# Kernel tuning notes

Hardware: AMD Instinct MI355X
Metric: run time of the kernel (lower is better)

Reference implementation:

```python
import jax, jax.numpy as jnp
import numpy as np

N_USERS = 100000
N_GAMES = 20000
D_USER = 128
D_GAME = 64
EMB = 64
H = 256
E = 1000000
S = 500000


def setup_inputs() -> dict:
    key = jax.random.key(0)
    ks = jax.random.split(key, 32)

    def w(k, fi, fo):
        return jax.random.normal(k, (fi, fo), jnp.float32) / np.float32(np.sqrt(fi))

    d_game_full = D_GAME + EMB  # game features concat game embedding
    inp = {
        "x_user": jax.random.normal(ks[0], (N_USERS, D_USER), jnp.float32),
        "x_game": jax.random.normal(ks[1], (N_GAMES, D_GAME), jnp.float32),
        "emb_game": jax.random.normal(ks[2], (N_GAMES, EMB), jnp.float32) * 0.1,
        "edge_weight_ug": jax.random.uniform(ks[3], (E,), jnp.float32),
        "edge_weight_gu": jax.random.uniform(ks[4], (E,), jnp.float32),
        "src_ug": jax.random.randint(ks[5], (E,), 0, N_USERS, jnp.int32),
        "dst_ug": jax.random.randint(ks[6], (E,), 0, N_GAMES, jnp.int32),
        "src_gu": jax.random.randint(ks[7], (E,), 0, N_GAMES, jnp.int32),
        "dst_gu": jax.random.randint(ks[8], (E,), 0, N_USERS, jnp.int32),
        "score_row": jax.random.randint(ks[9], (S,), 0, N_USERS, jnp.int32),
        "score_col": jax.random.randint(ks[10], (S,), 0, N_GAMES, jnp.int32),
    }
    # GraphConv params per layer per edge type: W_rel (messages), bias, W_root (self)
    dims = [(D_USER, d_game_full, H), (H, H, H), (H, H, H)]
    i = 11
    for l, (du, dg, out) in enumerate(dims, 1):
        inp[f"W_rel_ug{l}"] = w(ks[i], du, out); i += 1
        inp[f"b_ug{l}"] = jnp.zeros((out,), jnp.float32)
        inp[f"W_root_g{l}"] = w(ks[i], dg, out); i += 1
        inp[f"W_rel_gu{l}"] = w(ks[i], dg, out); i += 1
        inp[f"b_gu{l}"] = jnp.zeros((out,), jnp.float32)
        inp[f"W_root_u{l}"] = w(ks[i], du, out); i += 1
    return inp


def reference(x_user, x_game, emb_game, edge_weight_ug, edge_weight_gu,
              W_rel_ug1, b_ug1, W_root_g1, W_rel_gu1, b_gu1, W_root_u1,
              W_rel_ug2, b_ug2, W_root_g2, W_rel_gu2, b_gu2, W_root_u2,
              W_rel_ug3, b_ug3, W_root_g3, W_rel_gu3, b_gu3, W_root_u3,
              src_ug, dst_ug, src_gu, dst_gu, score_row, score_col):
    def conv(x_src, x_dst, src, dst, ew, Wr, br, Wo, n_dst):
        # GraphConv: sum_j w_ij * x_j -> lin_rel, plus lin_root(x_i)
        msg = jax.ops.segment_sum(x_src[src] * ew[:, None], dst, num_segments=n_dst)
        return msg @ Wr + br + x_dst @ Wo

    xu = x_user                                   # [Nu, 128]
    xg = jnp.concatenate([x_game, emb_game], axis=1)  # [Ng, 128]

    g = jax.nn.relu(conv(xu, xg, src_ug, dst_ug, edge_weight_ug, W_rel_ug1, b_ug1, W_root_g1, N_GAMES))
    u = jax.nn.relu(conv(xg, xu, src_gu, dst_gu, edge_weight_gu, W_rel_gu1, b_gu1, W_root_u1, N_USERS))

    g2 = jax.nn.relu(conv(u, g, src_ug, dst_ug, edge_weight_ug, W_rel_ug2, b_ug2, W_root_g2, N_GAMES))
    u2 = jax.nn.relu(conv(g, u, src_gu, dst_gu, edge_weight_gu, W_rel_gu2, b_gu2, W_root_u2, N_USERS))

    g3 = conv(u2, g2, src_ug, dst_ug, edge_weight_ug, W_rel_ug3, b_ug3, W_root_g3, N_GAMES)
    u3 = conv(g2, u2, src_gu, dst_gu, edge_weight_gu, W_rel_gu3, b_gu3, W_root_u3, N_USERS)
    # dropout(0.2) in eval mode is identity

    # DotProductEdgeDecoder
    return jnp.sum(u3[score_row] * g3[score_col], axis=1)  # [S]
```

## Files before the change

### kernel.cpp

```cpp
#include <hip/hip_runtime.h>

typedef unsigned short bf16_t;
typedef __attribute__((ext_vector_type(8))) short bf16x8;
typedef __attribute__((ext_vector_type(4))) float f32x4;

static constexpr int NU = 100000;
static constexpr int NG = 20000;
static constexpr int HD = 256;
static constexpr int EE = 1000000;
static constexpr int SS = 500000;

static constexpr int SH_G = 6,  SPAN_G = 64;
static constexpr int SH_U = 7,  SPAN_U = 128;
static constexpr int BKT_G = (NG + SPAN_G - 1) / SPAN_G;
static constexpr int BKT_U = (NU + SPAN_U - 1) / SPAN_U;
static constexpr int CAP_G = 4096;
static constexpr int CAP_U = 2048;
static constexpr int NBMAX = 1024;
static constexpr int PA_BLOCKS = 256;
static constexpr int PA_CHUNK = (EE + PA_BLOCKS - 1) / PA_BLOCKS;
static constexpr int TILE = 4096;

__device__ __forceinline__ float b2f(bf16_t u) {
    union { unsigned int i; float f; } x; x.i = ((unsigned int)u) << 16; return x.f;
}
__device__ __forceinline__ bf16_t f2b(float f) {
    union { float f; unsigned int i; } x; x.f = f;
    unsigned int r = x.i + 0x7FFF + ((x.i >> 16) & 1);
    return (bf16_t)(r >> 16);
}

__device__ __forceinline__ void accum8(float* acc, uint4 r, float w) {
    unsigned int u[4] = {r.x, r.y, r.z, r.w};
#pragma unroll
    for (int i = 0; i < 4; i++) {
        float lo = __uint_as_float(u[i] << 16);
        float hi = __uint_as_float(u[i] & 0xFFFF0000u);
        acc[2 * i]     = fmaf(w, lo, acc[2 * i]);
        acc[2 * i + 1] = fmaf(w, hi, acc[2 * i + 1]);
    }
}

__global__ void prep_feats(const float* __restrict__ xgame, const float* __restrict__ emb,
                           const float* __restrict__ xuser,
                           bf16_t* __restrict__ xg, bf16_t* __restrict__ xu,
                           int* __restrict__ gcg, int* __restrict__ gcu) {
    int id = blockIdx.x * 256 + threadIdx.x;
    if (id < BKT_G) gcg[id] = 0;
    if (id < BKT_U) gcu[id] = 0;
    const int ng4 = NG * 32;
    if (id < ng4) {
        int r = id >> 5, c = (id & 31) * 4;
        float4 v = (c < 64) ? *(const float4*)&xgame[(size_t)r * 64 + c]
                            : *(const float4*)&emb[(size_t)r * 64 + (c - 64)];
        ((ushort4*)xg)[id] = make_ushort4(f2b(v.x), f2b(v.y), f2b(v.z), f2b(v.w));
    } else {
        int j = id - ng4;
        if (j >= NU * 32) return;
        float4 v = ((const float4*)xuser)[j];
        ((ushort4*)xu)[j] = make_ushort4(f2b(v.x), f2b(v.y), f2b(v.z), f2b(v.w));
    }
}

struct WtArgs {
    const float* src[12];
    bf16_t* dst[12];
    int K[12];
    int off[13];
};
__global__ void wt_all(WtArgs a, int total) {
    int id = blockIdx.x * 256 + threadIdx.x;
    if (id >= total) return;
    int s = 0;
    while (id >= a.off[s + 1]) ++s;
    int local = id - a.off[s];
    int K = a.K[s];
    int k = local >> 8, n = local & 255;
    a.dst[s][(size_t)n * K + k] = f2b(a.src[s][local]);
}

__global__ __launch_bounds__(256) void chisto(const int* __restrict__ dug,
                                              const int* __restrict__ dgu,
                                              int* __restrict__ gcg, int* __restrict__ gcu) {
    __shared__ int cnt[NBMAX];
    int blk = blockIdx.x;
    int dir = blk >> 8, lb = blk & 255;
    const int* dst = dir ? dgu : dug;
    int* gc = dir ? gcu : gcg;
    int B = dir ? BKT_U : BKT_G;
    int sh = dir ? SH_U : SH_G;
    int t = threadIdx.x;
    for (int i = t; i < NBMAX; i += 256) cnt[i] = 0;
    __syncthreads();
    int beg = lb * PA_CHUNK, fin = min(EE, beg + PA_CHUNK);
    for (int i = beg + t; i < fin; i += 256)
        atomicAdd(&cnt[((unsigned)dst[i]) >> sh], 1);
    __syncthreads();
    for (int i = t; i < B; i += 256)
        if (cnt[i]) atomicAdd(&gc[i], cnt[i]);
}

__global__ void scan_coarse(const int* __restrict__ gcg, const int* __restrict__ gcu,
                            int* __restrict__ baseg, int* __restrict__ baseu,
                            int* __restrict__ gcurg, int* __restrict__ gcuru,
                            int* __restrict__ rpg, int* __restrict__ rpu) {
    if (blockIdx.x == 0 && threadIdx.x == 0) {
        int run = 0;
        for (int i = 0; i < BKT_G; i++) { baseg[i] = run; gcurg[i] = run; run += gcg[i]; }
        rpg[NG] = EE;
    } else if (blockIdx.x == 1 && threadIdx.x == 0) {
        int run = 0;
        for (int i = 0; i < BKT_U; i++) { baseu[i] = run; gcuru[i] = run; run += gcu[i]; }
        rpu[NU] = EE;
    }
}

__global__ __launch_bounds__(256) void passA(
    const int* __restrict__ sug, const int* __restrict__ dug, const float* __restrict__ wug,
    const int* __restrict__ sgu, const int* __restrict__ dgu, const float* __restrict__ wgu,
    int* __restrict__ gcurg, int* __restrict__ gcuru,
    int2* __restrict__ tmpG, int2* __restrict__ tmpU) {
    __shared__ int cnt[NBMAX], sscan[NBMAX], gb[NBMAX], sd[256];
    __shared__ unsigned short rankArr[TILE], sbkt[TILE];
    __shared__ int2 staged[TILE];
    int blk = blockIdx.x;
    int dir = blk >> 8, lb = blk & 255;
    const int* src = dir ? sgu : sug;
    const int* dst = dir ? dgu : dug;
    const float* w = dir ? wgu : wug;
    int* gcur = dir ? gcuru : gcurg;
    int2* tmp = dir ? tmpU : tmpG;
    int B = dir ? BKT_U : BKT_G;
    int sh = dir ? SH_U : SH_G;
    unsigned lmask = dir ? (SPAN_U - 1) : (SPAN_G - 1);
    int t = threadIdx.x;
    int beg = lb * PA_CHUNK, fin = min(EE, beg + PA_CHUNK);
    int n = fin - beg;
    for (int i = t; i < NBMAX; i += 256) cnt[i] = 0;
    __syncthreads();
    for (int i = t; i < n; i += 256) {
        int bkt = ((unsigned)dst[beg + i]) >> sh;
        rankArr[i] = (unsigned short)atomicAdd(&cnt[bkt], 1);
    }
    __syncthreads();
    {
        int v[4]; int s = 0;
#pragma unroll
        for (int j = 0; j < 4; j++) { v[j] = cnt[t * 4 + j]; s += v[j]; }
        sd[t] = s;
        __syncthreads();
        for (int off = 1; off < 256; off <<= 1) {
            int y = (t >= off) ? sd[t - off] : 0;
            __syncthreads();
            sd[t] += y;
            __syncthreads();
        }
        int run = sd[t] - s;
#pragma unroll
        for (int j = 0; j < 4; j++) { sscan[t * 4 + j] = run; run += v[j]; }
    }
    __syncthreads();
    for (int i = t; i < n; i += 256) {
        unsigned d = (unsigned)dst[beg + i];
        int bkt = d >> sh;
        int pos = sscan[bkt] + rankArr[i];
        staged[pos] = make_int2(src[beg + i] | ((d & lmask) << 17), __float_as_int(w[beg + i]));
        sbkt[pos] = (unsigned short)bkt;
    }
    __syncthreads();
    for (int i = t; i < B; i += 256)
        if (cnt[i]) gb[i] = atomicAdd(&gcur[i], cnt[i]);
    __syncthreads();
    for (int i = t; i < n; i += 256) {
        int bkt = sbkt[i];
        tmp[gb[bkt] + i - sscan[bkt]] = staged[i];
    }
}

template <int SPANB, int CAP>
__global__ __launch_bounds__(256) void passB(
    const int2* __restrict__ tmp, const int* __restrict__ base,
    int* __restrict__ rowptr, int2* __restrict__ eout, int B, int ntot) {
    __shared__ int cnt2[SPANB], lexcl[SPANB], cur[SPANB];
    __shared__ int2 staged[CAP];
    constexpr int KMAX = CAP / 256;
    int bkt = blockIdx.x;
    if (bkt >= B) return;
    int start = base[bkt];
    int end = (bkt == B - 1) ? EE : base[bkt + 1];
    int row0 = bkt * SPANB;
    int t = threadIdx.x;
    int count = end - start;
    if (count <= CAP) {
        for (int i = t; i < SPANB; i += 256) cnt2[i] = 0;
        __syncthreads();
        int2 e[KMAX]; int rk[KMAX];
#pragma unroll
        for (int k = 0; k < KMAX; k++) {
            int i = t + k * 256;
            if (i < count) {
                e[k] = tmp[start + i];
                rk[k] = atomicAdd(&cnt2[((unsigned)e[k].x) >> 17], 1);
            }
        }
        __syncthreads();
        if (t == 0) {
            int run = 0;
            for (int r = 0; r < SPANB; r++) { lexcl[r] = run; run += cnt2[r]; }
        }
        __syncthreads();
#pragma unroll
        for (int k = 0; k < KMAX; k++) {
            int i = t + k * 256;
            if (i < count) {
                int r = ((unsigned)e[k].x) >> 17;
                staged[lexcl[r] + rk[k]] = e[k];
            }
        }
        __syncthreads();
        for (int r = t; r < SPANB; r += 256) {
            int row = row0 + r;
            if (row < ntot) rowptr[row] = start + lexcl[r];
        }
        for (int i = t; i < count; i += 256) {
            int2 s = staged[i];
            eout[start + i] = make_int2(s.x & 0x1FFFF, s.y);
        }
    } else {
        for (int i = t; i < SPANB; i += 256) cnt2[i] = 0;
        __syncthreads();
        for (int i = start + t; i < end; i += 256)
            atomicAdd(&cnt2[((unsigned)tmp[i].x) >> 17], 1);
        __syncthreads();
        if (t == 0) {
            int run = 0;
            for (int r = 0; r < SPANB; r++) { int v = cnt2[r]; cur[r] = run; run += v; }
        }
        __syncthreads();
        for (int r = t; r < SPANB; r += 256) {
            int row = row0 + r;
            if (row < ntot) rowptr[row] = start + cur[r];
        }
        __syncthreads();
        for (int pos = start; pos < end; pos += CAP) {
            int n = min(CAP, end - pos);
            for (int i = t; i < SPANB; i += 256) cnt2[i] = 0;
            __syncthreads();
            int2 e[KMAX]; int rk[KMAX];
#pragma unroll
            for (int k = 0; k < KMAX; k++) {
                int i = t + k * 256;
                if (i < n) {
                    e[k] = tmp[pos + i];
                    rk[k] = atomicAdd(&cnt2[((unsigned)e[k].x) >> 17], 1);
                }
            }
            __syncthreads();
            if (t == 0) {
                int run = 0;
                for (int r = 0; r < SPANB; r++) { lexcl[r] = run; run += cnt2[r]; }
            }
            __syncthreads();
#pragma unroll
            for (int k = 0; k < KMAX; k++) {
                int i = t + k * 256;
                if (i < n) {
                    int r = ((unsigned)e[k].x) >> 17;
                    staged[lexcl[r] + rk[k]] = e[k];
                }
            }
            __syncthreads();
            for (int i = t; i < n; i += 256) {
                int2 s = staged[i];
                int r = ((unsigned)s.x) >> 17;
                int g = start + cur[r] + (i - lexcl[r]);
                eout[g] = make_int2(s.x & 0x1FFFF, s.y);
            }
            __syncthreads();
            for (int r = t; r < SPANB; r += 256) cur[r] += cnt2[r];
            __syncthreads();
        }
    }
}

template <int D>
__global__ __launch_bounds__(256) void seg_sum16(
    const bf16_t* __restrict__ feat, const int* __restrict__ rowptr,
    const int2* __restrict__ edges, bf16_t* __restrict__ out, int n_rows) {
    constexpr int LPE = D / 8;
    constexpr int EP = 64 / LPE;
    constexpr int UN = 4;
    int wid = (blockIdx.x * 256 + threadIdx.x) >> 6;
    int lane = threadIdx.x & 63;
    if (wid >= n_rows) return;
    int beg = rowptr[wid], end = rowptr[wid + 1];
    const int h = lane / LPE;
    const int cl = lane % LPE;
    const uint4* fb = (const uint4*)feat;
    float acc[8] = {};
    for (int eb = beg; eb < end; eb += UN * EP) {
        int2 ed[UN]; bool v[UN]; uint4 r[UN];
#pragma unroll
        for (int u = 0; u < UN; u++) {
            int e = eb + u * EP + h;
            v[u] = e < end;
            ed[u] = edges[v[u] ? e : beg];
        }
#pragma unroll
        for (int u = 0; u < UN; u++)
            r[u] = fb[(size_t)ed[u].x * (D / 8) + cl];
#pragma unroll
        for (int u = 0; u < UN; u++)
            accum8(acc, r[u], v[u] ? __int_as_float(ed[u].y) : 0.f);
    }
#pragma unroll
    for (int k = 0; k < 8; ++k) {
        acc[k] += __shfl_down(acc[k], 32, 64);
        if (LPE == 16) acc[k] += __shfl_down(acc[k], 16, 64);
    }
    if (lane < LPE) {
        uint4 o;
        o.x = (unsigned)f2b(acc[0]) | ((unsigned)f2b(acc[1]) << 16);
        o.y = (unsigned)f2b(acc[2]) | ((unsigned)f2b(acc[3]) << 16);
        o.z = (unsigned)f2b(acc[4]) | ((unsigned)f2b(acc[5]) << 16);
        o.w = (unsigned)f2b(acc[6]) | ((unsigned)f2b(acc[7]) << 16);
        ((uint4*)(out + (size_t)wid * D))[lane] = o;
    }
}

template <bool TWOPASS>
__global__ __launch_bounds__(256) void gemm_mfma(
    const bf16_t* __restrict__ A1, const bf16_t* __restrict__ W1t,
    const bf16_t* __restrict__ A2, const bf16_t* __restrict__ W2t,
    const float* __restrict__ bias, bf16_t* __restrict__ C,
    int M, int K, int addc, int relu) {
    constexpr int LS = 40;
    __shared__ bf16_t As[128 * LS];
    __shared__ bf16_t Bs[128 * LS];
    const int t = threadIdx.x;
    const int lane = t & 63, wave = t >> 6;
    const int wm = (wave >> 1) * 64, wn = (wave & 1) * 64;
    const int rowBase = blockIdx.x * 128;
    const int colBase = blockIdx.y * 128;
    const int lm = lane & 15;
    const int quad = lane >> 4;
    f32x4 acc[4][4] = {};

    const int npass = TWOPASS ? 2 : 1;
    for (int pass = 0; pass < npass; ++pass) {
        const bf16_t* A = pass ? A2 : A1;
        const bf16_t* Wt = pass ? W2t : W1t;
        for (int k0 = 0; k0 < K; k0 += 32) {
#pragma unroll
            for (int i = 0; i < 2; ++i) {
                int li = t + i * 256;
                int r = li >> 2, c = (li & 3) * 8;
                int gm = rowBase + r;
                bf16x8 v = {};
                if (gm < M) v = *(const bf16x8*)&A[(size_t)gm * K + k0 + c];
                *(bf16x8*)&As[r * LS + c] = v;
            }
#pragma unroll
            for (int i = 0; i < 2; ++i) {
                int li = t + i * 256;
                int r = li >> 2, c = (li & 3) * 8;
                bf16x8 v = *(const bf16x8*)&Wt[(size_t)(colBase + r) * K + k0 + c];
                *(bf16x8*)&Bs[r * LS + c] = v;
            }
            __syncthreads();
            bf16x8 af[4], bfr[4];
#pragma unroll
            for (int i = 0; i < 4; ++i)
                af[i] = *(const bf16x8*)&As[(wm + i * 16 + lm) * LS + quad * 8];
#pragma unroll
            for (int j = 0; j < 4; ++j)
                bfr[j] = *(const bf16x8*)&Bs[(wn + j * 16 + lm) * LS + quad * 8];
#pragma unroll
            for (int i = 0; i < 4; ++i)
#pragma unroll
                for (int j = 0; j < 4; ++j)
                    acc[i][j] = __builtin_amdgcn_mfma_f32_16x16x32_bf16(bfr[j], af[i], acc[i][j], 0, 0, 0);
            __syncthreads();
        }
    }

#pragma unroll
    for (int i = 0; i < 4; ++i) {
        int row = rowBase + wm + i * 16 + lm;
        if (row >= M) continue;
#pragma unroll
        for (int j = 0; j < 4; ++j) {
            int col = colBase + wn + j * 16 + quad * 4;
            float v0 = acc[i][j][0], v1 = acc[i][j][1], v2 = acc[i][j][2], v3 = acc[i][j][3];
            if (bias) {
                float4 b4 = *(const float4*)&bias[col];
                v0 += b4.x; v1 += b4.y; v2 += b4.z; v3 += b4.w;
            }
            bf16_t* cp = &C[(size_t)row * HD + col];
            if (addc) {
                ushort4 old = *(const ushort4*)cp;
                v0 += b2f(old.x); v1 += b2f(old.y); v2 += b2f(old.z); v3 += b2f(old.w);
            }
            if (relu) {
                v0 = fmaxf(v0, 0.f); v1 = fmaxf(v1, 0.f);
                v2 = fmaxf(v2, 0.f); v3 = fmaxf(v3, 0.f);
            }
            *(ushort4*)cp = make_ushort4(f2b(v0), f2b(v1), f2b(v2), f2b(v3));
        }
    }
}

__global__ __launch_bounds__(256) void decode2(
    const bf16_t* __restrict__ u3, const bf16_t* __restrict__ g3,
    const int* __restrict__ row, const int* __restrict__ col,
    float* __restrict__ out, int S) {
    int wid = (blockIdx.x * 256 + threadIdx.x) >> 6;
    int lane = threadIdx.x & 63;
    int p = wid * 2 + (lane >> 5);
    int cl = lane & 31;
    if (p >= S) p = S - 1;
    int r = row[p], c = col[p];
    uint4 a = ((const uint4*)(u3 + (size_t)r * 256))[cl];
    uint4 b = ((const uint4*)(g3 + (size_t)c * 256))[cl];
    float s = 0.f;
    unsigned ua[4] = {a.x, a.y, a.z, a.w}, ub[4] = {b.x, b.y, b.z, b.w};
#pragma unroll
    for (int i = 0; i < 4; i++) {
        float alo = __uint_as_float(ua[i] << 16), ahi = __uint_as_float(ua[i] & 0xFFFF0000u);
        float blo = __uint_as_float(ub[i] << 16), bhi = __uint_as_float(ub[i] & 0xFFFF0000u);
        s = fmaf(alo, blo, s);
        s = fmaf(ahi, bhi, s);
    }
#pragma unroll
    for (int d = 16; d > 0; d >>= 1) s += __shfl_down(s, d, 64);
    if (cl == 0) out[p] = s;
}

extern "C" void kernel_launch(void* const* d_in, const int* in_sizes, int n_in,
                              void* d_out, int out_size, void* d_ws, size_t ws_size,
                              hipStream_t stream) {
    const float* x_user  = (const float*)d_in[0];
    const float* x_game  = (const float*)d_in[1];
    const float* emb_game= (const float*)d_in[2];
    const float* ew_ug   = (const float*)d_in[3];
    const float* ew_gu   = (const float*)d_in[4];
    const int* src_ug    = (const int*)d_in[5];
    const int* dst_ug    = (const int*)d_in[6];
    const int* src_gu    = (const int*)d_in[7];
    const int* dst_gu    = (const int*)d_in[8];
    const int* score_row = (const int*)d_in[9];
    const int* score_col = (const int*)d_in[10];
    const float* Wr_ug[3] = {(const float*)d_in[11], (const float*)d_in[17], (const float*)d_in[23]};
    const float* b_ug[3]  = {(const float*)d_in[12], (const float*)d_in[18], (const float*)d_in[24]};
    const float* Wo_g[3]  = {(const float*)d_in[13], (const float*)d_in[19], (const float*)d_in[25]};
    const float* Wr_gu[3] = {(const float*)d_in[14], (const float*)d_in[20], (const float*)d_in[26]};
    const float* b_gu[3]  = {(const float*)d_in[15], (const float*)d_in[21], (const float*)d_in[27]};
    const float* Wo_u[3]  = {(const float*)d_in[16], (const float*)d_in[22], (const float*)d_in[28]};
    float* out = (float*)d_out;
    (void)in_sizes; (void)n_in; (void)out_size;

    constexpr size_t WS_NEEDED = 183500000;
    if (ws_size < WS_NEEDED) return;

    char* ws = (char*)d_ws;
    size_t off = 0;
    auto alloc = [&](size_t bytes) -> void* {
        void* p = ws + off;
        off += (bytes + 255) & ~(size_t)255;
        return p;
    };
    bf16_t* xg   = (bf16_t*)alloc((size_t)NG * 128 * 2);
    bf16_t* xu   = (bf16_t*)alloc((size_t)NU * 128 * 2);
    bf16_t* uA   = (bf16_t*)alloc((size_t)NU * HD * 2);
    bf16_t* uB   = (bf16_t*)alloc((size_t)NU * HD * 2);
    bf16_t* gA   = (bf16_t*)alloc((size_t)NG * HD * 2);
    bf16_t* gB   = (bf16_t*)alloc((size_t)NG * HD * 2);
    bf16_t* buf  = (bf16_t*)alloc((size_t)NG * HD * 2);
    int2*   e_ug = (int2*)  alloc((size_t)EE * 8);
    int2*   e_gu = (int2*)  alloc((size_t)EE * 8);
    bf16_t* WrugT[3], *WogT[3], *WrguT[3], *WouT[3];
    const int Ks[3] = {128, 256, 256};
    for (int l = 0; l < 3; ++l) {
        WrugT[l] = (bf16_t*)alloc((size_t)Ks[l] * HD * 2);
        WogT[l]  = (bf16_t*)alloc((size_t)Ks[l] * HD * 2);
        WrguT[l] = (bf16_t*)alloc((size_t)Ks[l] * HD * 2);
        WouT[l]  = (bf16_t*)alloc((size_t)Ks[l] * HD * 2);
    }
    int* rowptr_g = (int*)alloc((NG + 1) * 4);
    int* rowptr_u = (int*)alloc((NU + 1) * 4);
    int* gcnt_g   = (int*)alloc(BKT_G * 4);
    int* gcnt_u   = (int*)alloc(BKT_U * 4);
    int* base_g   = (int*)alloc(BKT_G * 4);
    int* base_u   = (int*)alloc(BKT_U * 4);
    int* gcur_g   = (int*)alloc(BKT_G * 4);
    int* gcur_u   = (int*)alloc(BKT_U * 4);
    int2* tmp_g = (int2*)uB;
    int2* tmp_u = tmp_g + EE;

    {
        int n4 = NG * 32 + NU * 32;
        prep_feats<<<(n4 + 255) / 256, 256, 0, stream>>>(x_game, emb_game, x_user, xg, xu,
                                                         gcnt_g, gcnt_u);
        WtArgs wa;
        const float* srcs[12] = {Wr_ug[0], Wo_g[0], Wr_gu[0], Wo_u[0],
                                 Wr_ug[1], Wo_g[1], Wr_gu[1], Wo_u[1],
                                 Wr_ug[2], Wo_g[2], Wr_gu[2], Wo_u[2]};
        bf16_t* dsts[12] = {WrugT[0], WogT[0], WrguT[0], WouT[0],
                            WrugT[1], WogT[1], WrguT[1], WouT[1],
                            WrugT[2], WogT[2], WrguT[2], WouT[2]};
        int total = 0;
        for (int i = 0; i < 12; ++i) {
            wa.src[i] = srcs[i]; wa.dst[i] = dsts[i];
            wa.K[i] = Ks[i / 4]; wa.off[i] = total;
            total += Ks[i / 4] * HD;
        }
        wa.off[12] = total;
        wt_all<<<(total + 255) / 256, 256, 0, stream>>>(wa, total);
    }
    chisto<<<2 * PA_BLOCKS, 256, 0, stream>>>(dst_ug, dst_gu, gcnt_g, gcnt_u);
    scan_coarse<<<2, 64, 0, stream>>>(gcnt_g, gcnt_u, base_g, base_u, gcur_g, gcur_u,
                                      rowptr_g, rowptr_u);
    passA<<<2 * PA_BLOCKS, 256, 0, stream>>>(src_ug, dst_ug, ew_ug, src_gu, dst_gu, ew_gu,
                                             gcur_g, gcur_u, tmp_g, tmp_u);
    passB<SPAN_G, CAP_G><<<BKT_G, 256, 0, stream>>>(tmp_g, base_g, rowptr_g, e_ug, BKT_G, NG);
    passB<SPAN_U, CAP_U><<<BKT_U, 256, 0, stream>>>(tmp_u, base_u, rowptr_u, e_gu, BKT_U, NU);

    const dim3 GG((NG + 127) / 128, 2), GU((NU + 127) / 128, 2);
    const int SEG_G = (NG + 3) / 4, SEG_U = (NU + 3) / 4;

    seg_sum16<128><<<SEG_G, 256, 0, stream>>>(xu, rowptr_g, e_ug, buf, NG);
    gemm_mfma<true><<<GG, 256, 0, stream>>>(buf, WrugT[0], xg, WogT[0], b_ug[0], gA, NG, 128, 0, 1);
    gemm_mfma<false><<<GG, 256, 0, stream>>>(xg, WrguT[0], nullptr, nullptr, nullptr, buf, NG, 128, 0, 0);
    seg_sum16<256><<<SEG_U, 256, 0, stream>>>(buf, rowptr_u, e_gu, uA, NU);
    gemm_mfma<false><<<GU, 256, 0, stream>>>(xu, WouT[0], nullptr, nullptr, b_gu[0], uA, NU, 128, 1, 1);

    seg_sum16<256><<<SEG_G, 256, 0, stream>>>(uA, rowptr_g, e_ug, buf, NG);
    gemm_mfma<true><<<GG, 256, 0, stream>>>(buf, WrugT[1], gA, WogT[1], b_ug[1], gB, NG, 256, 0, 1);
    gemm_mfma<false><<<GG, 256, 0, stream>>>(gA, WrguT[1], nullptr, nullptr, nullptr, buf, NG, 256, 0, 0);
    seg_sum16<256><<<SEG_U, 256, 0, stream>>>(buf, rowptr_u, e_gu, uB, NU);
    gemm_mfma<false><<<GU, 256, 0, stream>>>(uA, WouT[1], nullptr, nullptr, b_gu[1], uB, NU, 256, 1, 1);

    seg_sum16<256><<<SEG_G, 256, 0, stream>>>(uB, rowptr_g, e_ug, buf, NG);
    gemm_mfma<true><<<GG, 256, 0, stream>>>(buf, WrugT[2], gB, WogT[2], b_ug[2], gA, NG, 256, 0, 0);
    gemm_mfma<false><<<GG, 256, 0, stream>>>(gB, WrguT[2], nullptr, nullptr, nullptr, buf, NG, 256, 0, 0);
    seg_sum16<256><<<SEG_U, 256, 0, stream>>>(buf, rowptr_u, e_gu, uA, NU);
    gemm_mfma<false><<<GU, 256, 0, stream>>>(uB, WouT[2], nullptr, nullptr, b_gu[2], uA, NU, 256, 1, 0);

    decode2<<<((SS + 1) / 2 + 3) / 4, 256, 0, stream>>>(uA, gA, score_row, score_col, out, SS);
}
```

Measured before the change: 931.7 us.

## Fuse independent game-side GEMMs with segment-sum launches via block-index dispatch

Turns the segment-sum and GEMM kernels into device bodies and adds a combined kernel that sends the first blocks to a GEMM and the rest to a segment sum. Each game-side GEMM now runs concurrently with an independent aggregation in the same launch, with intermediate buffers reassigned to existing storage (gB and xu) to avoid write conflicts. The aim is to fill idle compute units during the small GEMMs and drop launch gaps. In exchange, segment-sum blocks inherit the GEMM's shared-memory and register footprint, which could lower their occupancy.

New measurement: 1.036 ms. 11.2% more time.

```diff
diff --git a/kernel.cpp b/kernel.cpp
--- a/kernel.cpp
+++ b/kernel.cpp
@@ -284,13 +284,13 @@
 }
 
 template <int D>
-__global__ __launch_bounds__(256) void seg_sum16(
+__device__ __forceinline__ void seg_body(
     const bf16_t* __restrict__ feat, const int* __restrict__ rowptr,
-    const int2* __restrict__ edges, bf16_t* __restrict__ out, int n_rows) {
+    const int2* __restrict__ edges, bf16_t* __restrict__ out, int n_rows, int blk) {
     constexpr int LPE = D / 8;
     constexpr int EP = 64 / LPE;
     constexpr int UN = 4;
-    int wid = (blockIdx.x * 256 + threadIdx.x) >> 6;
+    int wid = (blk * 256 + (int)threadIdx.x) >> 6;
     int lane = threadIdx.x & 63;
     if (wid >= n_rows) return;
     int beg = rowptr[wid], end = rowptr[wid + 1];
@@ -329,19 +329,19 @@
 }
 
 template <bool TWOPASS>
-__global__ __launch_bounds__(256) void gemm_mfma(
+__device__ __forceinline__ void gemm_body(
     const bf16_t* __restrict__ A1, const bf16_t* __restrict__ W1t,
     const bf16_t* __restrict__ A2, const bf16_t* __restrict__ W2t,
     const float* __restrict__ bias, bf16_t* __restrict__ C,
-    int M, int K, int addc, int relu) {
+    int M, int K, int addc, int relu, int bx, int by) {
     constexpr int LS = 40;
     __shared__ bf16_t As[128 * LS];
     __shared__ bf16_t Bs[128 * LS];
     const int t = threadIdx.x;
     const int lane = t & 63, wave = t >> 6;
     const int wm = (wave >> 1) * 64, wn = (wave & 1) * 64;
-    const int rowBase = blockIdx.x * 128;
-    const int colBase = blockIdx.y * 128;
+    const int rowBase = bx * 128;
+    const int colBase = by * 128;
     const int lm = lane & 15;
     const int quad = lane >> 4;
     f32x4 acc[4][4] = {};
@@ -408,6 +408,28 @@
             *(ushort4*)cp = make_ushort4(f2b(v0), f2b(v1), f2b(v2), f2b(v3));
         }
     }
+}
+
+template <bool TWOPASS>
+__global__ __launch_bounds__(256) void gemm_mfma(
+    const bf16_t* A1, const bf16_t* W1t, const bf16_t* A2, const bf16_t* W2t,
+    const float* bias, bf16_t* C, int M, int K, int addc, int relu) {
+    gemm_body<TWOPASS>(A1, W1t, A2, W2t, bias, C, M, K, addc, relu, blockIdx.x, blockIdx.y);
+}
+
+template <int D, bool TWOPASS>
+__global__ __launch_bounds__(256) void fused_gs(
+    const bf16_t* A1, const bf16_t* W1t, const bf16_t* A2, const bf16_t* W2t,
+    const float* bias, bf16_t* C, int M, int K, int addc, int relu,
+    int gemmBlocks, int gridM,
+    const bf16_t* feat, const int* rowptr, const int2* edges,
+    bf16_t* segOut, int n_rows) {
+    int b = blockIdx.x;
+    if (b < gemmBlocks)
+        gemm_body<TWOPASS>(A1, W1t, A2, W2t, bias, C, M, K, addc, relu,
+                           b % gridM, b / gridM);
+    else
+        seg_body<D>(feat, rowptr, edges, segOut, n_rows, b - gemmBlocks);
 }
 
 __global__ __launch_bounds__(256) void decode2(
@@ -496,6 +518,8 @@
     int* gcur_u   = (int*)alloc(BKT_U * 4);
     int2* tmp_g = (int2*)uB;
     int2* tmp_u = tmp_g + EE;
+    bf16_t* Ybuf1 = gB;
+    bf16_t* Ybuf23 = xu;
 
     {
         int n4 = NG * 32 + NU * 32;
@@ -525,26 +549,37 @@
     passB<SPAN_G, CAP_G><<<BKT_G, 256, 0, stream>>>(tmp_g, base_g, rowptr_g, e_ug, BKT_G, NG);
     passB<SPAN_U, CAP_U><<<BKT_U, 256, 0, stream>>>(tmp_u, base_u, rowptr_u, e_gu, BKT_U, NU);
 
-    const dim3 GG((NG + 127) / 128, 2), GU((NU + 127) / 128, 2);
+    const int GM_G = (NG + 127) / 128;
+    const int GB_G = GM_G * 2;
     const int SEG_G = (NG + 3) / 4, SEG_U = (NU + 3) / 4;
-
-    seg_sum16<128><<<SEG_G, 256, 0, stream>>>(xu, rowptr_g, e_ug, buf, NG);
-    gemm_mfma<true><<<GG, 256, 0, stream>>>(buf, WrugT[0], xg, WogT[0], b_ug[0], gA, NG, 128, 0, 1);
-    gemm_mfma<false><<<GG, 256, 0, stream>>>(xg, WrguT[0], nullptr, nullptr, nullptr, buf, NG, 128, 0, 0);
-    seg_sum16<256><<<SEG_U, 256, 0, stream>>>(buf, rowptr_u, e_gu, uA, NU);
-    gemm_mfma<false><<<GU, 256, 0, stream>>>(xu, WouT[0], nullptr, nullptr, b_gu[0], uA, NU, 128, 1, 1);
-
-    seg_sum16<256><<<SEG_G, 256, 0, stream>>>(uA, rowptr_g, e_ug, buf, NG);
-    gemm_mfma<true><<<GG, 256, 0, stream>>>(buf, WrugT[1], gA, WogT[1], b_ug[1], gB, NG, 256, 0, 1);
-    gemm_mfma<false><<<GG, 256, 0, stream>>>(gA, WrguT[1], nullptr, nullptr, nullptr, buf, NG, 256, 0, 0);
-    seg_sum16<256><<<SEG_U, 256, 0, stream>>>(buf, rowptr_u, e_gu, uB, NU);
-    gemm_mfma<false><<<GU, 256, 0, stream>>>(uA, WouT[1], nullptr, nullptr, b_gu[1], uB, NU, 256, 1, 1);
-
-    seg_sum16<256><<<SEG_G, 256, 0, stream>>>(uB, rowptr_g, e_ug, buf, NG);
-    gemm_mfma<true><<<GG, 256, 0, stream>>>(buf, WrugT[2], gB, WogT[2], b_ug[2], gA, NG, 256, 0, 0);
-    gemm_mfma<false><<<GG, 256, 0, stream>>>(gB, WrguT[2], nullptr, nullptr, nullptr, buf, NG, 256, 0, 0);
-    seg_sum16<256><<<SEG_U, 256, 0, stream>>>(buf, rowptr_u, e_gu, uA, NU);
-    gemm_mfma<false><<<GU, 256, 0, stream>>>(uB, WouT[2], nullptr, nullptr, b_gu[2], uA, NU, 256, 1, 0);
+    const dim3 GU((NU + 127) / 128, 2);
+
+    fused_gs<128, false><<<GB_G + SEG_G, 256, 0, stream>>>(
+        xg, WrguT[0], nullptr, nullptr, nullptr, Ybuf1, NG, 128, 0, 0, GB_G, GM_G,
+        xu, rowptr_g, e_ug, buf, NG);
+    fused_gs<256, true><<<GB_G + SEG_U, 256, 0, stream>>>(
+        buf, WrugT[0], xg, WogT[0], b_ug[0], gA, NG, 128, 0, 1, GB_G, GM_G,
+        Ybuf1, rowptr_u, e_gu, uA, NU);
+    gemm_mfma<false><<<GU, 256, 0, stream>>>(xu, WouT[0], nullptr, nullptr, b_gu[0],
+                                             uA, NU, 128, 1, 1);
+
+    fused_gs<256, false><<<GB_G + SEG_G, 256, 0, stream>>>(
+        gA, WrguT[1], nullptr, nullptr, nullptr, Ybuf23, NG, 256, 0, 0, GB_G, GM_G,
+        uA, rowptr_g, e_ug, buf, NG);
+    fused_gs<256, true><<<GB_G + SEG_U, 256, 0, stream>>>(
+        buf, WrugT[1], gA, WogT[1], b_ug[1], gB, NG, 256, 0, 1, GB_G, GM_G,
+        Ybuf23, rowptr_u, e_gu, uB, NU);
+    gemm_mfma<false><<<GU, 256, 0, stream>>>(uA, WouT[1], nullptr, nullptr, b_gu[1],
+                                             uB, NU, 256, 1, 1);
+
+    fused_gs<256, false><<<GB_G + SEG_G, 256, 0, stream>>>(
+        gB, WrguT[2], nullptr, nullptr, nullptr, Ybuf23, NG, 256, 0, 0, GB_G, GM_G,
+        uB, rowptr_g, e_ug, buf, NG);
+    fused_gs<256, true><<<GB_G + SEG_U, 256, 0, stream>>>(
+        buf, WrugT[2], gB, WogT[2], b_ug[2], gA, NG, 256, 0, 0, GB_G, GM_G,
+        Ybuf23, rowptr_u, e_gu, uA, NU);
+    gemm_mfma<false><<<GU, 256, 0, stream>>>(uB, WouT[2], nullptr, nullptr, b_gu[2],
+                                             uA, NU, 256, 1, 0);
 
     decode2<<<((SS + 1) / 2 + 3) / 4, 256, 0, stream>>>(uA, gA, score_row, score_col, out, SS);
 }
```
